# Kernel tuning notes

Measured on AMD Instinct MI355X. Metric: run time of the kernel, lower is better.

Reference implementation:

```python
import jax, jax.numpy as jnp
import numpy as np

B, C, H, W = 1024, 3, 224, 220
ROWS, COLS = 4, 5          # _factorize_patches(20)
P = ROWS * COLS            # num_patches = 20
HID = 32                   # FeatureNet hidden


def setup_inputs() -> dict:
    key = jax.random.key(0)
    kx, k1, k2, k3, k4 = jax.random.split(key, 5)
    x = jax.random.normal(kx, (B, C, H, W), dtype=jnp.float32)
    # per-patch FeatureNet params: Linear(1,HID) -> ReLU -> Linear(HID,1)
    lim1 = 1.0  # kaiming-uniform bound for fan_in=1 is sqrt(1/1); exact init unimportant
    w1 = jax.random.uniform(k1, (P, HID), jnp.float32, -lim1, lim1)
    b1 = jax.random.uniform(k2, (P, HID), jnp.float32, -lim1, lim1)
    lim2 = 1.0 / np.sqrt(HID)
    w2 = jax.random.uniform(k3, (P, HID), jnp.float32, -lim2, lim2)
    b2 = jax.random.uniform(k4, (P,), jnp.float32, -lim2, lim2)
    return {"x": x, "w1": w1, "b1": b1, "w2": w2, "b2": b2}


def reference(x, w1, b1, w2, b2):
    Bc = x.shape[0]
    ph, pw = H // ROWS, W // COLS
    # vectorized patch mean-pool over (C, ph, pw): [B, rows, cols] -> [B, P]
    xp = x.reshape(Bc, C, ROWS, ph, COLS, pw)
    feats = xp.mean(axis=(1, 3, 5)).reshape(Bc, P)  # [B, P]
    # per-patch scalar MLP: relu(f*w1 + b1) @ w2 + b2, batched over P
    h = jax.nn.relu(feats[:, :, None] * w1[None] + b1[None])  # [B, P, HID]
    contribs = jnp.einsum('bph,ph->bp', h, w2) + b2[None]      # [B, P]
    score = contribs.sum(axis=1, keepdims=True)                # [B, 1]
    return score, contribs
```

## Files before the change

### kernel.cpp

```cpp
#include <hip/hip_runtime.h>

#define CCH 3
#define HH 224
#define WW 220
#define ROWS 4
#define COLS 5
#define NP 20
#define HID 32
#define PH 56
#define PW 44

#define W4      (WW / 4)
#define IMG4    (CCH * HH * W4)
#define LPP     (W4 / COLS)
#define INV_N   (1.0f / 7392.0f)

#define NWAVES  8
#define JITER   (PH / NWAVES)

typedef float v4f __attribute__((ext_vector_type(4)));

__global__ __launch_bounds__(512) void fused_patch_nam_kernel(
    const float* __restrict__ x,
    const float* __restrict__ w1, const float* __restrict__ b1,
    const float* __restrict__ w2, const float* __restrict__ b2,
    float* __restrict__ out, int B)
{
    const int b    = blockIdx.x;
    const int tid  = threadIdx.x;
    const int wid  = tid >> 6;
    const int lane = tid & 63;

    const v4f* img4 = (const v4f*)x + (size_t)b * IMG4;

    float part[ROWS] = {0.f, 0.f, 0.f, 0.f};

    if (lane < W4) {
        for (int c = 0; c < CCH; ++c) {
            const v4f* pbase = img4 + (size_t)(c * HH + wid) * W4 + lane;
            #pragma unroll
            for (int j = 0; j < JITER; ++j) {
                const v4f* rb = pbase + (j * NWAVES) * W4;
                #pragma unroll
                for (int pr = 0; pr < ROWS; ++pr) {
                    v4f v = __builtin_nontemporal_load(rb + pr * PH * W4);
                    part[pr] += (v.x + v.y) + (v.z + v.w);
                }
            }
        }
    }

    __shared__ float red[NWAVES][ROWS][W4 + 1];
    if (lane < W4) {
        #pragma unroll
        for (int pr = 0; pr < ROWS; ++pr)
            red[wid][pr][lane] = part[pr];
    }
    __syncthreads();

    __shared__ float contribs_s[NP];
    if (tid < NP) {
        const int pr = tid / COLS;
        const int pc = tid - pr * COLS;
        float s = 0.f;
        #pragma unroll
        for (int w = 0; w < NWAVES; ++w)
            #pragma unroll
            for (int l = 0; l < LPP; ++l)
                s += red[w][pr][pc * LPP + l];
        const float f = s * INV_N;

        float acc = 0.f;
        #pragma unroll
        for (int k = 0; k < HID; ++k) {
            float h = fmaf(f, w1[tid * HID + k], b1[tid * HID + k]);
            acc = fmaf(fmaxf(h, 0.f), w2[tid * HID + k], acc);
        }
        const float contrib = acc + b2[tid];
        out[B + (size_t)b * NP + tid] = contrib;
        contribs_s[tid] = contrib;
    }
    __syncthreads();

    if (tid == 0) {
        float s = 0.f;
        #pragma unroll
        for (int p = 0; p < NP; ++p) s += contribs_s[p];
        out[b] = s;
    }
}

extern "C" void kernel_launch(void* const* d_in, const int* in_sizes, int n_in,
                              void* d_out, int out_size, void* d_ws, size_t ws_size,
                              hipStream_t stream)
{
    const float* x  = (const float*)d_in[0];
    const float* w1 = (const float*)d_in[1];
    const float* b1 = (const float*)d_in[2];
    const float* w2 = (const float*)d_in[3];
    const float* b2 = (const float*)d_in[4];
    float* out = (float*)d_out;

    const int B = in_sizes[0] / (CCH * HH * WW);

    fused_patch_nam_kernel<<<B, 512, 0, stream>>>(x, w1, b1, w2, b2, out, B);
}
```

Baseline: 731.0 us.

## Stream image linearly with all threads and bin sums into per-thread LDS histograms

Each thread now reads contiguous groups of eight float4 values across the flattened image, instead of having only 55 of 64 lanes active reading row-strided chunks. Each thread computes which patch bin its group belongs to using multiply-shift division and accumulates partial sums into private per-thread shared-memory bins, splitting at most at one column boundary. The bins are then reduced with wave shuffles. This keeps every lane busy and makes the load stream contiguous, at the cost of 40KB of LDS per block, which may lower occupancy, plus extra index arithmetic.

New measurement: 895.6 us. 22.5% more time.

```diff
diff --git a/kernel.cpp b/kernel.cpp
--- a/kernel.cpp
+++ b/kernel.cpp
@@ -3,89 +3,136 @@
 #define CCH 3
 #define HH 224
 #define WW 220
-#define ROWS 4
-#define COLS 5
 #define NP 20
 #define HID 32
-#define PH 56
-#define PW 44
 
-#define W4      (WW / 4)
-#define IMG4    (CCH * HH * W4)
-#define LPP     (W4 / COLS)
-#define INV_N   (1.0f / 7392.0f)
-
-#define NWAVES  8
-#define JITER   (PH / NWAVES)
+#define W4     (WW / 4)
+#define IMG4   (CCH * HH * W4)
+#define NT     512
+#define GPT    8
+#define NGRP   (IMG4 / GPT)
+#define FULLIT (NGRP / NT)
+#define TAILT  (NGRP - FULLIT*NT)
+#define INV_N  (1.0f / 7392.0f)
 
 typedef float v4f __attribute__((ext_vector_type(4)));
 
-__global__ __launch_bounds__(512) void fused_patch_nam_kernel(
+__device__ __forceinline__ unsigned bin_of(unsigned idx, unsigned &c4, unsigned &pc)
+{
+    unsigned row = (idx * 38131u) >> 21;
+    c4 = idx - row * 55u;
+    unsigned h = row >= 224u ? row - 224u : row;
+    h = h >= 224u ? h - 224u : h;
+    unsigned pr = (h * 293u) >> 14;
+    pc = (c4 * 94u) >> 10;
+    return pr * 5u + pc;
+}
+
+__global__ __launch_bounds__(NT) void fused_patch_nam_kernel(
     const float* __restrict__ x,
     const float* __restrict__ w1, const float* __restrict__ b1,
     const float* __restrict__ w2, const float* __restrict__ b2,
     float* __restrict__ out, int B)
 {
-    const int b    = blockIdx.x;
-    const int tid  = threadIdx.x;
-    const int wid  = tid >> 6;
-    const int lane = tid & 63;
+    const int b   = blockIdx.x;
+    const int tid = threadIdx.x;
+
+    __shared__ float bins[NP * NT];
+
+    #pragma unroll
+    for (int i = 0; i < NP; ++i) bins[i * NT + tid] = 0.f;
+    __syncthreads();
 
     const v4f* img4 = (const v4f*)x + (size_t)b * IMG4;
 
-    float part[ROWS] = {0.f, 0.f, 0.f, 0.f};
+    auto process = [&](unsigned g) {
+        const unsigned idx0 = g * GPT;
+        const v4f* p = img4 + idx0;
+        v4f a[GPT];
+        #pragma unroll
+        for (int i = 0; i < GPT; ++i)
+            a[i] = __builtin_nontemporal_load(p + i);
 
-    if (lane < W4) {
-        for (int c = 0; c < CCH; ++c) {
-            const v4f* pbase = img4 + (size_t)(c * HH + wid) * W4 + lane;
-            #pragma unroll
-            for (int j = 0; j < JITER; ++j) {
-                const v4f* rb = pbase + (j * NWAVES) * W4;
-                #pragma unroll
-                for (int pr = 0; pr < ROWS; ++pr) {
-                    v4f v = __builtin_nontemporal_load(rb + pr * PH * W4);
-                    part[pr] += (v.x + v.y) + (v.z + v.w);
-                }
-            }
+        unsigned c40, pc0, c47, pc7;
+        const unsigned bin0 = bin_of(idx0,             c40, pc0);
+        const unsigned bin7 = bin_of(idx0 + (GPT - 1), c47, pc7);
+
+        float v[GPT];
+        #pragma unroll
+        for (int i = 0; i < GPT; ++i)
+            v[i] = (a[i].x + a[i].y) + (a[i].z + a[i].w);
+
+        const unsigned nb = pc0 * 11u + 11u;
+        float sa = v[0];
+        float sb = v[GPT - 1];
+        #pragma unroll
+        for (int i = 1; i < GPT - 1; ++i) {
+            const bool past = (c40 + (unsigned)i) >= nb;
+            sa += past ? 0.f : v[i];
+            sb += past ? v[i] : 0.f;
         }
+        bins[bin0 * NT + tid] += sa;
+        bins[bin7 * NT + tid] += sb;
+    };
+
+    for (int it = 0; it < FULLIT; ++it)
+        process((unsigned)(it * NT + tid));
+    if (tid < TAILT)
+        process((unsigned)(FULLIT * NT + tid));
+    __syncthreads();
+
+    const int wid = tid >> 6, lane = tid & 63;
+    float wsum0 = 0.f, wsum1 = 0.f, wsum2 = 0.f;
+    {
+        float s = 0.f;
+        #pragma unroll
+        for (int k = 0; k < 8; ++k) s += bins[wid * NT + lane + k * 64];
+        #pragma unroll
+        for (int off = 32; off >= 1; off >>= 1) s += __shfl_xor(s, off, 64);
+        wsum0 = s;
     }
-
-    __shared__ float red[NWAVES][ROWS][W4 + 1];
-    if (lane < W4) {
+    {
+        float s = 0.f;
         #pragma unroll
-        for (int pr = 0; pr < ROWS; ++pr)
-            red[wid][pr][lane] = part[pr];
+        for (int k = 0; k < 8; ++k) s += bins[(wid + 8) * NT + lane + k * 64];
+        #pragma unroll
+        for (int off = 32; off >= 1; off >>= 1) s += __shfl_xor(s, off, 64);
+        wsum1 = s;
+    }
+    if (wid < 4) {
+        float s = 0.f;
+        #pragma unroll
+        for (int k = 0; k < 8; ++k) s += bins[(wid + 16) * NT + lane + k * 64];
+        #pragma unroll
+        for (int off = 32; off >= 1; off >>= 1) s += __shfl_xor(s, off, 64);
+        wsum2 = s;
+    }
+    __syncthreads();
+    if (lane == 0) {
+        bins[wid]     = wsum0;
+        bins[wid + 8] = wsum1;
+        if (wid < 4) bins[wid + 16] = wsum2;
     }
     __syncthreads();
 
-    __shared__ float contribs_s[NP];
     if (tid < NP) {
-        const int pr = tid / COLS;
-        const int pc = tid - pr * COLS;
-        float s = 0.f;
-        #pragma unroll
-        for (int w = 0; w < NWAVES; ++w)
-            #pragma unroll
-            for (int l = 0; l < LPP; ++l)
-                s += red[w][pr][pc * LPP + l];
-        const float f = s * INV_N;
-
+        const float f = bins[tid] * INV_N;
         float acc = 0.f;
         #pragma unroll
         for (int k = 0; k < HID; ++k) {
-            float h = fmaf(f, w1[tid * HID + k], b1[tid * HID + k]);
-            acc = fmaf(fmaxf(h, 0.f), w2[tid * HID + k], acc);
+            const float hh = fmaf(f, w1[tid * HID + k], b1[tid * HID + k]);
+            acc = fmaf(fmaxf(hh, 0.f), w2[tid * HID + k], acc);
         }
         const float contrib = acc + b2[tid];
         out[B + (size_t)b * NP + tid] = contrib;
-        contribs_s[tid] = contrib;
+        bins[64 + tid] = contrib;
     }
     __syncthreads();
 
     if (tid == 0) {
         float s = 0.f;
         #pragma unroll
-        for (int p = 0; p < NP; ++p) s += contribs_s[p];
+        for (int p = 0; p < NP; ++p) s += bins[64 + p];
         out[b] = s;
     }
 }
@@ -103,5 +150,5 @@
 
     const int B = in_sizes[0] / (CCH * HH * WW);
 
-    fused_patch_nam_kernel<<<B, 512, 0, stream>>>(x, w1, b1, w2, b2, out, B);
+    fused_patch_nam_kernel<<<B, NT, 0, stream>>>(x, w1, b1, w2, b2, out, B);
 }
```
